# Performance work log

Hardware: AMD Instinct MI355X
Metric: run time of the kernel (lower is better)

## Reference

```python
import jax, jax.numpy as jnp
import numpy as np

N = 50000      # nodes
E = 800000     # edges
G = 2000       # graphs
F_IN = 34
HID = 256
H = 8
D = 32         # HID // H
L = 5


def _layer_norm(x, g, b, eps=1e-5):
    m = x.mean(-1, keepdims=True)
    v = ((x - m) ** 2).mean(-1, keepdims=True)
    return (x - m) / jnp.sqrt(v + eps) * g + b


def _gelu(x):
    return jax.nn.gelu(x, approximate=False)  # torch exact GELU


def _segment_softmax(scores, seg, n):
    # scores: [E', H], seg: [E'] target node ids
    m = jax.ops.segment_max(scores, seg, num_segments=n)
    m = jnp.where(jnp.isfinite(m), m, 0.0)
    ex = jnp.exp(scores - m[seg])
    den = jax.ops.segment_sum(ex, seg, num_segments=n)
    return ex / (den[seg] + 1e-16)


def setup_inputs() -> dict:
    key = jax.random.key(0)
    ks = iter(jax.random.split(key, 64))

    def p(shape, fan):
        return (jax.random.normal(next(ks), shape, jnp.float32) / np.sqrt(fan)).astype(jnp.float32)

    inp = {}
    inp['x'] = jax.random.normal(next(ks), (N, F_IN), jnp.float32)
    inp['edge_index'] = jax.random.randint(next(ks), (2, E), 0, N, jnp.int32)
    inp['batch'] = jnp.sort(jax.random.randint(next(ks), (N,), 0, G, jnp.int32))

    # input embed
    inp['in_W'] = p((F_IN, HID), F_IN); inp['in_b'] = jnp.zeros((HID,), jnp.float32)
    inp['in_ln_g'] = jnp.ones((HID,), jnp.float32); inp['in_ln_b'] = jnp.zeros((HID,), jnp.float32)
    # 5 GATv2 layers (stacked on leading dim)
    inp['gat_Wl'] = p((L, HID, HID), HID); inp['gat_bl'] = jnp.zeros((L, HID), jnp.float32)
    inp['gat_Wr'] = p((L, HID, HID), HID); inp['gat_br'] = jnp.zeros((L, HID), jnp.float32)
    inp['gat_att'] = p((L, H, D), D)
    inp['gat_bias'] = jnp.zeros((L, HID), jnp.float32)
    inp['gat_ln_g'] = jnp.ones((L, HID), jnp.float32); inp['gat_ln_b'] = jnp.zeros((L, HID), jnp.float32)
    # TransformerConv
    inp['tr_Wq'] = p((HID, HID), HID); inp['tr_bq'] = jnp.zeros((HID,), jnp.float32)
    inp['tr_Wk'] = p((HID, HID), HID); inp['tr_bk'] = jnp.zeros((HID,), jnp.float32)
    inp['tr_Wv'] = p((HID, HID), HID); inp['tr_bv'] = jnp.zeros((HID,), jnp.float32)
    inp['tr_Wskip'] = p((HID, HID), HID); inp['tr_bskip'] = jnp.zeros((HID,), jnp.float32)
    inp['tr_ln_g'] = jnp.ones((HID,), jnp.float32); inp['tr_ln_b'] = jnp.zeros((HID,), jnp.float32)
    # output proj
    inp['out_W'] = p((2 * HID, 2 * HID), 2 * HID); inp['out_b'] = jnp.zeros((2 * HID,), jnp.float32)
    inp['out_ln_g'] = jnp.ones((2 * HID,), jnp.float32); inp['out_ln_b'] = jnp.zeros((2 * HID,), jnp.float32)
    return inp


def reference(x, edge_index, batch,
              in_W, in_b, in_ln_g, in_ln_b,
              gat_Wl, gat_bl, gat_Wr, gat_br, gat_att, gat_bias, gat_ln_g, gat_ln_b,
              tr_Wq, tr_bq, tr_Wk, tr_bk, tr_Wv, tr_bv, tr_Wskip, tr_bskip, tr_ln_g, tr_ln_b,
              out_W, out_b, out_ln_g, out_ln_b):
    # input embedding (dropout inactive in eval)
    h = _gelu(_layer_norm(x @ in_W + in_b, in_ln_g, in_ln_b))

    src, dst = edge_index[0], edge_index[1]  # PyG: row=source j, col=target i
    loops = jnp.arange(N, dtype=src.dtype)
    s2 = jnp.concatenate([src, loops])  # GATv2 adds self loops
    d2 = jnp.concatenate([dst, loops])

    for l in range(L):  # small fixed loop over layers
        xl = (h @ gat_Wl[l] + gat_bl[l]).reshape(N, H, D)  # source transform / message
        xr = (h @ gat_Wr[l] + gat_br[l]).reshape(N, H, D)  # target transform
        e = jax.nn.leaky_relu(xl[s2] + xr[d2], 0.2)        # [E', H, D]
        score = jnp.einsum('ehd,hd->eh', e, gat_att[l])
        alpha = _segment_softmax(score, d2, N)             # softmax over incoming edges
        out = jax.ops.segment_sum(xl[s2] * alpha[..., None], d2, num_segments=N)
        out = out.reshape(N, HID) + gat_bias[l]
        h = h + _gelu(_layer_norm(out, gat_ln_g[l], gat_ln_b[l]))

    # TransformerConv (no self loops, root_weight skip connection)
    q = (h @ tr_Wq + tr_bq).reshape(N, H, D)
    k = (h @ tr_Wk + tr_bk).reshape(N, H, D)
    v = (h @ tr_Wv + tr_bv).reshape(N, H, D)
    score = (q[dst] * k[src]).sum(-1) / jnp.sqrt(jnp.float32(D))  # [E, H]
    alpha = _segment_softmax(score, dst, N)
    out = jax.ops.segment_sum(v[src] * alpha[..., None], dst, num_segments=N).reshape(N, HID)
    out = out + h @ tr_Wskip + tr_bskip
    h = h + _layer_norm(out, tr_ln_g, tr_ln_b)

    # global mean + max pool
    cnt = jax.ops.segment_sum(jnp.ones((N,), h.dtype), batch, num_segments=G)
    h_mean = jax.ops.segment_sum(h, batch, num_segments=G) / jnp.maximum(cnt, 1.0)[:, None]
    h_max = jax.ops.segment_max(h, batch, num_segments=G)
    h_max = jnp.where(jnp.isfinite(h_max), h_max, 0.0)
    ge = jnp.concatenate([h_mean, h_max], axis=-1)  # [G, 512]
    return _gelu(_layer_norm(ge @ out_W + out_b, out_ln_g, out_ln_b))
```

## Files before the change

### kernel.cpp

```cpp
#include <hip/hip_runtime.h>
#include <math.h>

#define N_NODES 50000
#define N_EDGES 800000
#define N_GRAPH 2000
#define F_INPUT 34
#define HID 256
#define NLAYER 5

typedef __attribute__((ext_vector_type(8))) short short8;
typedef __attribute__((ext_vector_type(4))) float float4v;

__device__ __forceinline__ float gelu_f(float x) {
  return 0.5f * x * (1.0f + erff(x * 0.70710678118654752440f));
}
__device__ __forceinline__ unsigned short bfr(float f) {
  unsigned u = __float_as_uint(f);
  return (unsigned short)((u + 0x7fffu + ((u >> 16) & 1u)) >> 16);
}
__device__ __forceinline__ float b2f(unsigned short s) {
  return __uint_as_float(((unsigned)s) << 16);
}
__device__ __forceinline__ float4 ld4bf(const unsigned short* p) {
  ushort4 u = *(const ushort4*)p;
  float4 f;
  f.x = b2f(u.x); f.y = b2f(u.y); f.z = b2f(u.z); f.w = b2f(u.w);
  return f;
}
__device__ __forceinline__ void acp16(const unsigned short* g, unsigned short* l) {
  __builtin_amdgcn_global_load_lds(
      (const __attribute__((address_space(1))) void*)g,
      (__attribute__((address_space(3))) void*)l, 16, 0, 0);
}

__global__ __launch_bounds__(256) void gemm_bias(
    const float* __restrict__ A, const float* __restrict__ B,
    const float* __restrict__ bias, float* __restrict__ C,
    int M, int Nn, int K) {
  __shared__ float As[16][64];
  __shared__ float Bs[16][64];
  int tid = threadIdx.x;
  int tx = tid & 15, ty = tid >> 4;
  int row0 = blockIdx.y * 64;
  int col0 = blockIdx.x * 64;
  float acc[4][4] = {};
  int a_r = tid >> 2;
  int a_c = (tid & 3) * 4;
  int b_r = tid >> 4;
  int b_c = (tid & 15) * 4;

  for (int k0 = 0; k0 < K; k0 += 16) {
    int ar = row0 + a_r;
#pragma unroll
    for (int i = 0; i < 4; ++i) {
      int kc = k0 + a_c + i;
      As[a_c + i][a_r] = (ar < M && kc < K) ? A[(long)ar * K + kc] : 0.f;
    }
    int bk = k0 + b_r;
    if (bk < K) {
      float4 bv = *(const float4*)&B[(long)bk * Nn + col0 + b_c];
      Bs[b_r][b_c + 0] = bv.x; Bs[b_r][b_c + 1] = bv.y;
      Bs[b_r][b_c + 2] = bv.z; Bs[b_r][b_c + 3] = bv.w;
    } else {
      Bs[b_r][b_c + 0] = 0.f; Bs[b_r][b_c + 1] = 0.f;
      Bs[b_r][b_c + 2] = 0.f; Bs[b_r][b_c + 3] = 0.f;
    }
    __syncthreads();
#pragma unroll
    for (int kk = 0; kk < 16; ++kk) {
      float4 a = *(const float4*)&As[kk][ty * 4];
      float4 b = *(const float4*)&Bs[kk][tx * 4];
      float av[4] = {a.x, a.y, a.z, a.w};
      float bv[4] = {b.x, b.y, b.z, b.w};
#pragma unroll
      for (int i = 0; i < 4; ++i)
#pragma unroll
        for (int j = 0; j < 4; ++j) acc[i][j] += av[i] * bv[j];
    }
    __syncthreads();
  }
  float4 bi = *(const float4*)&bias[col0 + tx * 4];
  float bia[4] = {bi.x, bi.y, bi.z, bi.w};
#pragma unroll
  for (int i = 0; i < 4; ++i) {
    int r = row0 + ty * 4 + i;
    if (r < M) {
      float4 o;
      o.x = acc[i][0] + bia[0]; o.y = acc[i][1] + bia[1];
      o.z = acc[i][2] + bia[2]; o.w = acc[i][3] + bia[3];
      *(float4*)&C[(long)r * Nn + col0 + tx * 4] = o;
    }
  }
}

__global__ __launch_bounds__(256) void gemm_mfma(
    const unsigned short* __restrict__ A, const unsigned short* __restrict__ Bt,
    const float* __restrict__ bias, void* __restrict__ Cv,
    int M, int Nn, int K, int flags) {
  __shared__ unsigned short smem[12288];
  unsigned short* As = smem;
  unsigned short* Bs = smem + 4096;
  int tid = threadIdx.x;
  int wave = tid >> 6, lane = tid & 63;
  int row0 = blockIdx.y * 128;
  int col0 = blockIdx.x * 128;
  int wm0 = (wave >> 1) * 64;
  int wn0 = (wave & 1) * 64;
  int q = lane >> 4;
  int ln = lane & 15;

  int srow = wave * 16 + (lane >> 2);
  int scol = (lane & 3) * 8;
  int ra0 = min(row0 + srow, M - 1);
  int ra1 = min(row0 + srow + 64, M - 1);
  const unsigned short* pa0 = A + (size_t)ra0 * K + scol;
  const unsigned short* pa1 = A + (size_t)ra1 * K + scol;
  const unsigned short* pb0 = Bt + (size_t)(col0 + srow) * K + scol;
  const unsigned short* pb1 = Bt + (size_t)(col0 + srow + 64) * K + scol;
  unsigned short* la0 = As + wave * 512;
  unsigned short* la1 = As + wave * 512 + 2048;
  unsigned short* lb0 = Bs + wave * 512;
  unsigned short* lb1 = Bs + wave * 512 + 2048;

  float4v acc[4][4];
#pragma unroll
  for (int i = 0; i < 4; ++i)
#pragma unroll
    for (int j = 0; j < 4; ++j) acc[i][j] = (float4v)0.f;

  for (int k0 = 0; k0 < K; k0 += 32) {
    acp16(pa0 + k0, la0);
    acp16(pa1 + k0, la1);
    acp16(pb0 + k0, lb0);
    acp16(pb1 + k0, lb1);
    __syncthreads();
    short8 af[4], bf[4];
#pragma unroll
    for (int i = 0; i < 4; ++i)
      af[i] = *(const short8*)&As[(wm0 + i * 16 + ln) * 32 + q * 8];
#pragma unroll
    for (int j = 0; j < 4; ++j)
      bf[j] = *(const short8*)&Bs[(wn0 + j * 16 + ln) * 32 + q * 8];
#pragma unroll
    for (int i = 0; i < 4; ++i)
#pragma unroll
      for (int j = 0; j < 4; ++j)
        acc[i][j] = __builtin_amdgcn_mfma_f32_16x16x32_bf16(af[i], bf[j], acc[i][j], 0, 0, 0);
    __syncthreads();
  }
  int rb = (lane >> 4) * 4;
  if (flags & 2) {
    unsigned short* Cb = (unsigned short*)Cv;
    unsigned short* eb = smem + wave * 2560;
#pragma unroll
    for (int p = 0; p < 2; ++p) {
#pragma unroll
      for (int jj = 0; jj < 2; ++jj) {
        int j = p * 2 + jj;
        float bv = bias[col0 + wn0 + j * 16 + ln];
#pragma unroll
        for (int i = 0; i < 4; ++i)
#pragma unroll
          for (int r = 0; r < 4; ++r)
            eb[(i * 16 + rb + r) * 40 + jj * 16 + ln] = bfr(acc[i][j][r] + bv);
      }
      int grow = row0 + wm0 + lane;
      uint4 w0 = *(uint4*)&eb[lane * 40 + 0];
      uint4 w1 = *(uint4*)&eb[lane * 40 + 8];
      uint4 w2 = *(uint4*)&eb[lane * 40 + 16];
      uint4 w3 = *(uint4*)&eb[lane * 40 + 24];
      if (grow < M) {
        unsigned short* dst = Cb + (size_t)grow * Nn + col0 + wn0 + p * 32;
        *(uint4*)&dst[0] = w0;
        *(uint4*)&dst[8] = w1;
        *(uint4*)&dst[16] = w2;
        *(uint4*)&dst[24] = w3;
      }
    }
  } else {
    float* C = (float*)Cv;
#pragma unroll
    for (int j = 0; j < 4; ++j) {
      int col = col0 + wn0 + j * 16 + ln;
      float bv = bias[col];
#pragma unroll
      for (int i = 0; i < 4; ++i)
#pragma unroll
        for (int r = 0; r < 4; ++r) {
          int row = row0 + wm0 + i * 16 + rb + r;
          if (row < M) C[(size_t)row * Nn + col] = acc[i][j][r] + bv;
        }
    }
  }
}

__global__ __launch_bounds__(256) void prep_w(
    const float* __restrict__ Wl, const float* __restrict__ Wr,
    const float* __restrict__ Wq, const float* __restrict__ Wk,
    const float* __restrict__ Wv, const float* __restrict__ Wsk,
    unsigned short* __restrict__ out) {
  __shared__ float t[32][33];
  int m = blockIdx.z;
  const float* W = (m < 10) ? (((m & 1) ? Wr : Wl) + (size_t)(m >> 1) * 65536)
                 : (m == 10) ? Wq : (m == 11) ? Wk : (m == 12) ? Wv : Wsk;
  int k0 = blockIdx.y * 32, n0 = blockIdx.x * 32;
  int r = threadIdx.x >> 5, c = threadIdx.x & 31;
  for (int rr = r; rr < 32; rr += 8)
    t[rr][c] = W[(size_t)(k0 + rr) * HID + n0 + c];
  __syncthreads();
  unsigned short* o = out + (size_t)m * 65536;
  for (int rr = r; rr < 32; rr += 8)
    o[(size_t)(n0 + rr) * HID + k0 + c] = bfr(t[c][rr]);
}

__global__ __launch_bounds__(256) void prep_wout(const float* __restrict__ W,
                                                 unsigned short* __restrict__ o) {
  __shared__ float t[32][33];
  int k0 = blockIdx.y * 32, n0 = blockIdx.x * 32;
  int r = threadIdx.x >> 5, c = threadIdx.x & 31;
  for (int rr = r; rr < 32; rr += 8)
    t[rr][c] = W[(size_t)(k0 + rr) * 512 + n0 + c];
  __syncthreads();
  for (int rr = r; rr < 32; rr += 8)
    o[(size_t)(n0 + rr) * 512 + k0 + c] = bfr(t[c][rr]);
}

__global__ __launch_bounds__(256) void prep_bias(
    const float* __restrict__ bl, const float* __restrict__ br,
    const float* __restrict__ bq, const float* __restrict__ bk,
    const float* __restrict__ bv, float* __restrict__ out) {
  int i = blockIdx.x * 256 + threadIdx.x;
  if (i < 2560) {
    int l = i >> 9, c = i & 511;
    out[i] = (c < 256) ? bl[l * 256 + c] : br[l * 256 + (c - 256)];
  } else if (i < 3328) {
    int j = i - 2560;
    out[i] = (j < 256) ? bq[j] : (j < 512) ? bk[j - 256] : bv[j - 512];
  }
}

__global__ __launch_bounds__(256) void ln_act(
    const float* __restrict__ in, const float* __restrict__ gam,
    const float* __restrict__ bet, float* __restrict__ out,
    unsigned short* __restrict__ outb,
    int n_rows, int width, int do_gelu) {
  int wid = blockIdx.x * 4 + (threadIdx.x >> 6);
  int lane = threadIdx.x & 63;
  if (wid >= n_rows) return;
  int chunks = width >> 8;
  float4 v[2];
  float s = 0.f;
  for (int c = 0; c < chunks; ++c) {
    int off = c * 256 + lane * 4;
    float4 t = *(const float4*)&in[(size_t)wid * width + off];
    v[c] = t;
    s += t.x + t.y + t.z + t.w;
  }
  for (int o = 1; o < 64; o <<= 1) s += __shfl_xor(s, o);
  float mean = s / (float)width;
  float vs = 0.f;
  for (int c = 0; c < chunks; ++c) {
    float dx = v[c].x - mean, dy = v[c].y - mean, dz = v[c].z - mean, dw = v[c].w - mean;
    vs += dx * dx + dy * dy + dz * dz + dw * dw;
  }
  for (int o = 1; o < 64; o <<= 1) vs += __shfl_xor(vs, o);
  float inv = rsqrtf(vs / (float)width + 1e-5f);
  for (int c = 0; c < chunks; ++c) {
    int off = c * 256 + lane * 4;
    float4 g4 = *(const float4*)&gam[off];
    float4 b4 = *(const float4*)&bet[off];
    float y[4] = {(v[c].x - mean) * inv * g4.x + b4.x,
                  (v[c].y - mean) * inv * g4.y + b4.y,
                  (v[c].z - mean) * inv * g4.z + b4.z,
                  (v[c].w - mean) * inv * g4.w + b4.w};
    if (do_gelu) {
#pragma unroll
      for (int i = 0; i < 4; ++i) y[i] = gelu_f(y[i]);
    }
    size_t idx = (size_t)wid * width + off;
    float4 o4 = {y[0], y[1], y[2], y[3]};
    *(float4*)&out[idx] = o4;
    if (outb) {
      ushort4 ob = {bfr(y[0]), bfr(y[1]), bfr(y[2]), bfr(y[3])};
      *(ushort4*)&outb[idx] = ob;
    }
  }
}

__global__ __launch_bounds__(256) void edge_count(const int* __restrict__ ei,
                                                  int* __restrict__ counts) {
  int e = blockIdx.x * 256 + threadIdx.x;
  if (e < N_EDGES) atomicAdd(&counts[ei[N_EDGES + e]], 1);
}

__global__ __launch_bounds__(1024) void scan1(const int* __restrict__ counts,
                                              int* __restrict__ indptr,
                                              int* __restrict__ bsums, int n) {
  __shared__ int sm[1024];
  int tid = threadIdx.x;
  int i = blockIdx.x * 1024 + tid;
  int v = (i < n) ? counts[i] : 0;
  sm[tid] = v;
  __syncthreads();
  for (int off = 1; off < 1024; off <<= 1) {
    int t = (tid >= off) ? sm[tid - off] : 0;
    __syncthreads();
    sm[tid] += t;
    __syncthreads();
  }
  if (i < n) indptr[i] = sm[tid] - v;
  if (tid == 1023) bsums[blockIdx.x] = sm[1023];
}

__global__ void scan2(int* __restrict__ bsums, int nb) {
  if (threadIdx.x == 0 && blockIdx.x == 0) {
    int acc = 0;
    for (int i = 0; i < nb; ++i) { int t = bsums[i]; bsums[i] = acc; acc += t; }
  }
}

__global__ __launch_bounds__(256) void scan3(const int* __restrict__ bsums,
                                             int* __restrict__ indptr,
                                             int* __restrict__ cursor, int n) {
  int i = blockIdx.x * 256 + threadIdx.x;
  if (i < n) {
    int v = indptr[i] + bsums[i >> 10];
    indptr[i] = v;
    cursor[i] = v;
  }
  if (i == 0) indptr[n] = N_EDGES;
}

__global__ __launch_bounds__(256) void edge_scatter(const int* __restrict__ ei,
                                                    int* __restrict__ cursor,
                                                    int* __restrict__ esrc) {
  int e = blockIdx.x * 256 + threadIdx.x;
  if (e < N_EDGES) {
    int d = ei[N_EDGES + e];
    int p = atomicAdd(&cursor[d], 1);
    esrc[p] = ei[e];
  }
}

#define GAT_EDGE(f)                                                        \
  {                                                                        \
    float ex = f.x + xri.x; ex = ex > 0.f ? ex : 0.2f * ex;                \
    float ey = f.y + xri.y; ey = ey > 0.f ? ey : 0.2f * ey;                \
    float ez = f.z + xri.z; ez = ez > 0.f ? ez : 0.2f * ez;                \
    float ew = f.w + xri.w; ew = ew > 0.f ? ew : 0.2f * ew;                \
    float p = ex * a4.x + ey * a4.y + ez * a4.z + ew * a4.w;               \
    p += __shfl_xor(p, 1); p += __shfl_xor(p, 2); p += __shfl_xor(p, 4);   \
    float wgt = __expf(fminf(p - m0, 60.f));                               \
    ax += wgt * f.x; ay += wgt * f.y; az += wgt * f.z; aw += wgt * f.w;    \
    lsum += wgt;                                                           \
  }

__global__ __launch_bounds__(256) void gat_agg(
    const unsigned short* __restrict__ xlr, const float* __restrict__ att,
    const int* __restrict__ indptr, const int* __restrict__ esrc,
    const float* __restrict__ pre_bias, const float* __restrict__ gam,
    const float* __restrict__ bet, float* __restrict__ h,
    unsigned short* __restrict__ hb) {
  int wid = blockIdx.x * 4 + (threadIdx.x >> 6);
  int lane = threadIdx.x & 63;
  if (wid >= N_NODES) return;
  size_t idx = (size_t)wid * HID + lane * 4;
  float4 pb = *(const float4*)&pre_bias[lane * 4];
  float4 g4 = *(const float4*)&gam[lane * 4];
  float4 b4 = *(const float4*)&bet[lane * 4];
  float4 r4 = *(const float4*)&h[idx];
  float4 xri = ld4bf(&xlr[(size_t)wid * 512 + 256 + lane * 4]);
  float4 a4 = *(const float4*)&att[lane * 4];
  int beg = indptr[wid], end = indptr[wid + 1];

  float m0, lsum, ax, ay, az, aw;
  {
    float4 f = ld4bf(&xlr[(size_t)wid * 512 + lane * 4]);
    float ex = f.x + xri.x; ex = ex > 0.f ? ex : 0.2f * ex;
    float ey = f.y + xri.y; ey = ey > 0.f ? ey : 0.2f * ey;
    float ez = f.z + xri.z; ez = ez > 0.f ? ez : 0.2f * ez;
    float ew = f.w + xri.w; ew = ew > 0.f ? ew : 0.2f * ew;
    float p = ex * a4.x + ey * a4.y + ez * a4.z + ew * a4.w;
    p += __shfl_xor(p, 1); p += __shfl_xor(p, 2); p += __shfl_xor(p, 4);
    m0 = p; lsum = 1.f;
    ax = f.x; ay = f.y; az = f.z; aw = f.w;
  }
  int e = beg;
  for (; e + 7 < end; e += 8) {
    int j0 = esrc[e],     j1 = esrc[e + 1], j2 = esrc[e + 2], j3 = esrc[e + 3];
    int j4 = esrc[e + 4], j5 = esrc[e + 5], j6 = esrc[e + 6], j7 = esrc[e + 7];
    float4 f0 = ld4bf(&xlr[(size_t)j0 * 512 + lane * 4]);
    float4 f1 = ld4bf(&xlr[(size_t)j1 * 512 + lane * 4]);
    float4 f2 = ld4bf(&xlr[(size_t)j2 * 512 + lane * 4]);
    float4 f3 = ld4bf(&xlr[(size_t)j3 * 512 + lane * 4]);
    float4 f4 = ld4bf(&xlr[(size_t)j4 * 512 + lane * 4]);
    float4 f5 = ld4bf(&xlr[(size_t)j5 * 512 + lane * 4]);
    float4 f6 = ld4bf(&xlr[(size_t)j6 * 512 + lane * 4]);
    float4 f7 = ld4bf(&xlr[(size_t)j7 * 512 + lane * 4]);
    GAT_EDGE(f0); GAT_EDGE(f1); GAT_EDGE(f2); GAT_EDGE(f3);
    GAT_EDGE(f4); GAT_EDGE(f5); GAT_EDGE(f6); GAT_EDGE(f7);
  }
  for (; e + 3 < end; e += 4) {
    int j0 = esrc[e], j1 = esrc[e + 1], j2 = esrc[e + 2], j3 = esrc[e + 3];
    float4 f0 = ld4bf(&xlr[(size_t)j0 * 512 + lane * 4]);
    float4 f1 = ld4bf(&xlr[(size_t)j1 * 512 + lane * 4]);
    float4 f2 = ld4bf(&xlr[(size_t)j2 * 512 + lane * 4]);
    float4 f3 = ld4bf(&xlr[(size_t)j3 * 512 + lane * 4]);
    GAT_EDGE(f0); GAT_EDGE(f1); GAT_EDGE(f2); GAT_EDGE(f3);
  }
  for (; e < end; ++e) {
    int j = esrc[e];
    float4 f = ld4bf(&xlr[(size_t)j * 512 + lane * 4]);
    GAT_EDGE(f);
  }
  float inv = 1.f / (lsum + 1e-16f);
  float y0 = ax * inv + pb.x, y1 = ay * inv + pb.y;
  float y2 = az * inv + pb.z, y3 = aw * inv + pb.w;
  float s = y0 + y1 + y2 + y3;
  for (int o = 1; o < 64; o <<= 1) s += __shfl_xor(s, o);
  float mean = s * (1.f / 256.f);
  float d0 = y0 - mean, d1 = y1 - mean, d2 = y2 - mean, d3 = y3 - mean;
  float vs = d0 * d0 + d1 * d1 + d2 * d2 + d3 * d3;
  for (int o = 1; o < 64; o <<= 1) vs += __shfl_xor(vs, o);
  float inv2 = rsqrtf(vs * (1.f / 256.f) + 1e-5f);
  y0 = gelu_f(d0 * inv2 * g4.x + b4.x) + r4.x;
  y1 = gelu_f(d1 * inv2 * g4.y + b4.y) + r4.y;
  y2 = gelu_f(d2 * inv2 * g4.z + b4.z) + r4.z;
  y3 = gelu_f(d3 * inv2 * g4.w + b4.w) + r4.w;
  float4 o4 = {y0, y1, y2, y3};
  *(float4*)&h[idx] = o4;
  ushort4 ob = {bfr(y0), bfr(y1), bfr(y2), bfr(y3)};
  *(ushort4*)&hb[idx] = ob;
}

#define TR_EDGE(kj, vj)                                                    \
  {                                                                        \
    float p = qi.x * kj.x + qi.y * kj.y + qi.z * kj.z + qi.w * kj.w;       \
    p += __shfl_xor(p, 1); p += __shfl_xor(p, 2); p += __shfl_xor(p, 4);   \
    float wgt = __expf(fminf(p * scale, 60.f));                            \
    ax += wgt * vj.x; ay += wgt * vj.y; az += wgt * vj.z; aw += wgt * vj.w;\
    lsum += wgt;                                                           \
  }

__global__ __launch_bounds__(256) void tr_agg(
    const unsigned short* __restrict__ qkv, const int* __restrict__ indptr,
    const int* __restrict__ esrc, const unsigned short* __restrict__ skipb,
    const float* __restrict__ gam, const float* __restrict__ bet,
    float* __restrict__ h) {
  int wid = blockIdx.x * 4 + (threadIdx.x >> 6);
  int lane = threadIdx.x & 63;
  if (wid >= N_NODES) return;
  size_t idx = (size_t)wid * HID + lane * 4;
  float4 sk = ld4bf(&skipb[idx]);
  float4 g4 = *(const float4*)&gam[lane * 4];
  float4 b4 = *(const float4*)&bet[lane * 4];
  float4 r4 = *(const float4*)&h[idx];
  float4 qi = ld4bf(&qkv[(size_t)wid * 768 + lane * 4]);
  int beg = indptr[wid], end = indptr[wid + 1];
  float lsum = 0.f;
  float ax = 0.f, ay = 0.f, az = 0.f, aw = 0.f;
  const float scale = 0.17677669529663687f;
  int e = beg;
  for (; e + 3 < end; e += 4) {
    int j0 = esrc[e], j1 = esrc[e + 1], j2 = esrc[e + 2], j3 = esrc[e + 3];
    float4 k0 = ld4bf(&qkv[(size_t)j0 * 768 + 256 + lane * 4]);
    float4 v0 = ld4bf(&qkv[(size_t)j0 * 768 + 512 + lane * 4]);
    float4 k1 = ld4bf(&qkv[(size_t)j1 * 768 + 256 + lane * 4]);
    float4 v1 = ld4bf(&qkv[(size_t)j1 * 768 + 512 + lane * 4]);
    float4 k2 = ld4bf(&qkv[(size_t)j2 * 768 + 256 + lane * 4]);
    float4 v2 = ld4bf(&qkv[(size_t)j2 * 768 + 512 + lane * 4]);
    float4 k3 = ld4bf(&qkv[(size_t)j3 * 768 + 256 + lane * 4]);
    float4 v3 = ld4bf(&qkv[(size_t)j3 * 768 + 512 + lane * 4]);
    TR_EDGE(k0, v0); TR_EDGE(k1, v1); TR_EDGE(k2, v2); TR_EDGE(k3, v3);
  }
  for (; e < end; ++e) {
    int j = esrc[e];
    float4 kj = ld4bf(&qkv[(size_t)j * 768 + 256 + lane * 4]);
    float4 vj = ld4bf(&qkv[(size_t)j * 768 + 512 + lane * 4]);
    TR_EDGE(kj, vj);
  }
  float inv = 1.f / (lsum + 1e-16f);
  float y0 = ax * inv + sk.x, y1 = ay * inv + sk.y;
  float y2 = az * inv + sk.z, y3 = aw * inv + sk.w;
  float s = y0 + y1 + y2 + y3;
  for (int o = 1; o < 64; o <<= 1) s += __shfl_xor(s, o);
  float mean = s * (1.f / 256.f);
  float d0 = y0 - mean, d1 = y1 - mean, d2 = y2 - mean, d3 = y3 - mean;
  float vs = d0 * d0 + d1 * d1 + d2 * d2 + d3 * d3;
  for (int o = 1; o < 64; o <<= 1) vs += __shfl_xor(vs, o);
  float inv2 = rsqrtf(vs * (1.f / 256.f) + 1e-5f);
  float4 o4;
  o4.x = r4.x + d0 * inv2 * g4.x + b4.x;
  o4.y = r4.y + d1 * inv2 * g4.y + b4.y;
  o4.z = r4.z + d2 * inv2 * g4.z + b4.z;
  o4.w = r4.w + d3 * inv2 * g4.w + b4.w;
  *(float4*)&h[idx] = o4;
}

__global__ __launch_bounds__(256) void graph_bounds(const int* __restrict__ batch,
                                                    int* __restrict__ gptr) {
  int i = blockIdx.x * 256 + threadIdx.x;
  if (i >= N_NODES) return;
  int b0 = batch[i];
  if (i == 0)
    for (int g = 0; g <= b0; ++g) gptr[g] = 0;
  int b1 = (i + 1 < N_NODES) ? batch[i + 1] : N_GRAPH;
  for (int g = b0 + 1; g <= b1; ++g) gptr[g] = i + 1;
}

__global__ __launch_bounds__(256) void pool_seg(
    const float* __restrict__ h, const int* __restrict__ gptr,
    unsigned short* __restrict__ geb) {
  int g = blockIdx.x, c = threadIdx.x;
  int s = gptr[g], e = gptr[g + 1];
  float sum = 0.f, mx = -INFINITY;
  for (int r = s; r < e; ++r) {
    float vv = h[(size_t)r * HID + c];
    sum += vv;
    mx = fmaxf(mx, vv);
  }
  int cnt = e - s;
  geb[(size_t)g * 512 + c] = bfr(sum / (float)max(cnt, 1));
  geb[(size_t)g * 512 + 256 + c] = bfr(cnt ? mx : 0.f);
}

static inline void mfma_launch(const unsigned short* A, const unsigned short* Bt,
                               const float* bias, void* C, int M, int Nn, int K,
                               int flags, hipStream_t s) {
  dim3 grid(Nn / 128, (M + 127) / 128);
  gemm_mfma<<<grid, 256, 0, s>>>(A, Bt, bias, C, M, Nn, K, flags);
}

extern "C" void kernel_launch(void* const* d_in, const int* in_sizes, int n_in,
                              void* d_out, int out_size, void* d_ws, size_t ws_size,
                              hipStream_t stream) {
  const float* x       = (const float*)d_in[0];
  const int*   ei      = (const int*)d_in[1];
  const int*   batch   = (const int*)d_in[2];
  const float* in_W    = (const float*)d_in[3];
  const float* in_b    = (const float*)d_in[4];
  const float* in_ln_g = (const float*)d_in[5];
  const float* in_ln_b = (const float*)d_in[6];
  const float* gat_Wl  = (const float*)d_in[7];
  const float* gat_bl  = (const float*)d_in[8];
  const float* gat_Wr  = (const float*)d_in[9];
  const float* gat_br  = (const float*)d_in[10];
  const float* gat_att = (const float*)d_in[11];
  const float* gat_bias= (const float*)d_in[12];
  const float* gat_ln_g= (const float*)d_in[13];
  const float* gat_ln_b= (const float*)d_in[14];
  const float* tr_Wq   = (const float*)d_in[15];
  const float* tr_bq   = (const float*)d_in[16];
  const float* tr_Wk   = (const float*)d_in[17];
  const float* tr_bk   = (const float*)d_in[18];
  const float* tr_Wv   = (const float*)d_in[19];
  const float* tr_bv   = (const float*)d_in[20];
  const float* tr_Wsk  = (const float*)d_in[21];
  const float* tr_bsk  = (const float*)d_in[22];
  const float* tr_ln_g = (const float*)d_in[23];
  const float* tr_ln_b = (const float*)d_in[24];
  const float* out_W   = (const float*)d_in[25];
  const float* out_b   = (const float*)d_in[26];
  const float* out_ln_g= (const float*)d_in[27];
  const float* out_ln_b= (const float*)d_in[28];

  char* w = (char*)d_ws;
  auto take = [&](size_t bytes) -> char* {
    char* p = w;
    w += (bytes + 255) & ~(size_t)255;
    return p;
  };
  const size_t NB = (size_t)N_NODES * HID * sizeof(float);
  float* h    = (float*)take(NB);
  float* aggO = (float*)take(NB);
  unsigned short* hb  = (unsigned short*)take((size_t)N_NODES * HID * 2);
  unsigned short* xq  = (unsigned short*)take((size_t)N_NODES * 768 * 2);
  unsigned short* wbuf= (unsigned short*)take((size_t)(14 * 65536 + 262144) * 2);
  float* bcat = (float*)take(3328 * sizeof(float));
  int* indptr = (int*)take((N_NODES + 1) * sizeof(int));
  int* cursor = (int*)take(N_NODES * sizeof(int));
  int* counts = (int*)take(N_NODES * sizeof(int));
  int* esrc   = (int*)take(N_EDGES * sizeof(int));
  int* bsums  = (int*)take(64 * sizeof(int));
  unsigned short* skipb = (unsigned short*)aggO;
  char* w2 = (char*)xq;
  auto take2 = [&](size_t bytes) -> char* {
    char* p = w2;
    w2 += (bytes + 255) & ~(size_t)255;
    return p;
  };
  int* gptr = (int*)take2((N_GRAPH + 1) * sizeof(int));
  unsigned short* geb = (unsigned short*)take2((size_t)N_GRAPH * 512 * 2);
  float* tbuf = (float*)take2((size_t)N_GRAPH * 512 * sizeof(float));

  const int EB = (N_EDGES + 255) / 256;
  const int WB = (N_NODES + 3) / 4;
  const int NSB = (N_NODES + 1023) / 1024;

  {
    dim3 g(8, 8, 14);
    prep_w<<<g, 256, 0, stream>>>(gat_Wl, gat_Wr, tr_Wq, tr_Wk, tr_Wv, tr_Wsk, wbuf);
    dim3 g2(16, 16);
    prep_wout<<<g2, 256, 0, stream>>>(out_W, wbuf + (size_t)14 * 65536);
    prep_bias<<<13, 256, 0, stream>>>(gat_bl, gat_br, tr_bq, tr_bk, tr_bv, bcat);
  }

  hipMemsetAsync(counts, 0, N_NODES * sizeof(int), stream);
  edge_count<<<EB, 256, 0, stream>>>(ei, counts);
  scan1<<<NSB, 1024, 0, stream>>>(counts, indptr, bsums, N_NODES);
  scan2<<<1, 64, 0, stream>>>(bsums, NSB);
  scan3<<<(N_NODES + 255) / 256, 256, 0, stream>>>(bsums, indptr, cursor, N_NODES);
  edge_scatter<<<EB, 256, 0, stream>>>(ei, cursor, esrc);

  {
    dim3 grid(HID / 64, (N_NODES + 63) / 64);
    gemm_bias<<<grid, 256, 0, stream>>>(x, in_W, in_b, aggO, N_NODES, HID, F_INPUT);
  }
  ln_act<<<WB, 256, 0, stream>>>(aggO, in_ln_g, in_ln_b, h, hb, N_NODES, HID, 1);

  for (int l = 0; l < NLAYER; ++l) {
    mfma_launch(hb, wbuf + (size_t)(2 * l) * 65536, bcat + l * 512, xq,
                N_NODES, 512, HID, 2, stream);
    gat_agg<<<WB, 256, 0, stream>>>(xq, gat_att + l * HID, indptr, esrc,
                                    gat_bias + l * HID, gat_ln_g + l * HID,
                                    gat_ln_b + l * HID, h, hb);
  }

  mfma_launch(hb, wbuf + (size_t)13 * 65536, tr_bsk, skipb,
              N_NODES, HID, HID, 2, stream);
  mfma_launch(hb, wbuf + (size_t)10 * 65536, bcat + 2560, xq,
              N_NODES, 768, HID, 2, stream);
  tr_agg<<<WB, 256, 0, stream>>>(xq, indptr, esrc, skipb, tr_ln_g, tr_ln_b, h);

  graph_bounds<<<(N_NODES + 255) / 256, 256, 0, stream>>>(batch, gptr);
  pool_seg<<<N_GRAPH, 256, 0, stream>>>(h, gptr, geb);

  mfma_launch(geb, wbuf + (size_t)14 * 65536, out_b, tbuf,
              N_GRAPH, 512, 512, 0, stream);
  ln_act<<<(N_GRAPH + 3) / 4, 256, 0, stream>>>(tbuf, out_ln_g, out_ln_b,
                                                (float*)d_out, nullptr,
                                                N_GRAPH, 512, 1);
}
```

Before: 1.274 ms.

## Interleave K/V weights, split transformer edges across wave pairs, drop tiny kernels

Reorders the K and V weight rows and biases so each lane's K and V values for a source node sit together, letting one 16-byte load fetch both. Each node in tr_agg is now handled by two waves that take alternate edges and combine partial sums through shared memory. The separate scan2 and graph_bounds kernels are removed: scan3 sums the block totals itself, and pool_seg finds graph bounds by binary search over batch. Loads of the LN, bias and residual parameters in gat_agg are moved after the edge loop to shorten register live ranges. The price is an extra block barrier in tr_agg and redundant bound searches across blocks.

```diff
diff --git a/kernel.cpp b/kernel.cpp
--- a/kernel.cpp
+++ b/kernel.cpp
@@ -26,6 +26,10 @@
   float4 f;
   f.x = b2f(u.x); f.y = b2f(u.y); f.z = b2f(u.z); f.w = b2f(u.w);
   return f;
+}
+__device__ __forceinline__ void unpk(unsigned u, float& a, float& b) {
+  a = __uint_as_float(u << 16);
+  b = __uint_as_float(u & 0xffff0000u);
 }
 __device__ __forceinline__ void acp16(const unsigned short* g, unsigned short* l) {
   __builtin_amdgcn_global_load_lds(
@@ -208,9 +212,22 @@
   for (int rr = r; rr < 32; rr += 8)
     t[rr][c] = W[(size_t)(k0 + rr) * HID + n0 + c];
   __syncthreads();
-  unsigned short* o = out + (size_t)m * 65536;
-  for (int rr = r; rr < 32; rr += 8)
-    o[(size_t)(n0 + rr) * HID + k0 + c] = bfr(t[c][rr]);
+  for (int rr = r; rr < 32; rr += 8) {
+    int n = n0 + rr;
+    unsigned short* o;
+    int drow;
+    if (m == 11) {
+      o = out + (size_t)10 * 65536;
+      drow = 256 + (n >> 2) * 8 + (n & 3);
+    } else if (m == 12) {
+      o = out + (size_t)10 * 65536;
+      drow = 256 + (n >> 2) * 8 + 4 + (n & 3);
+    } else {
+      o = out + (size_t)m * 65536;
+      drow = n;
+    }
+    o[(size_t)drow * HID + k0 + c] = bfr(t[c][rr]);
+  }
 }
 
 __global__ __launch_bounds__(256) void prep_wout(const float* __restrict__ W,
@@ -235,7 +252,12 @@
     out[i] = (c < 256) ? bl[l * 256 + c] : br[l * 256 + (c - 256)];
   } else if (i < 3328) {
     int j = i - 2560;
-    out[i] = (j < 256) ? bq[j] : (j < 512) ? bk[j - 256] : bv[j - 512];
+    if (j < 256) {
+      out[i] = bq[j];
+    } else {
+      int t = j - 256, g = t >> 3, r = t & 7;
+      out[i] = (r < 4) ? bk[4 * g + r] : bv[4 * g + (r - 4)];
+    }
   }
 }
 
@@ -312,19 +334,15 @@
   if (tid == 1023) bsums[blockIdx.x] = sm[1023];
 }
 
-__global__ void scan2(int* __restrict__ bsums, int nb) {
-  if (threadIdx.x == 0 && blockIdx.x == 0) {
-    int acc = 0;
-    for (int i = 0; i < nb; ++i) { int t = bsums[i]; bsums[i] = acc; acc += t; }
-  }
-}
-
 __global__ __launch_bounds__(256) void scan3(const int* __restrict__ bsums,
                                              int* __restrict__ indptr,
                                              int* __restrict__ cursor, int n) {
   int i = blockIdx.x * 256 + threadIdx.x;
+  int blk = blockIdx.x >> 2;
+  int off = 0;
+  for (int b = 0; b < blk; ++b) off += bsums[b];
   if (i < n) {
-    int v = indptr[i] + bsums[i >> 10];
+    int v = indptr[i] + off;
     indptr[i] = v;
     cursor[i] = v;
   }
@@ -364,11 +382,6 @@
   int wid = blockIdx.x * 4 + (threadIdx.x >> 6);
   int lane = threadIdx.x & 63;
   if (wid >= N_NODES) return;
-  size_t idx = (size_t)wid * HID + lane * 4;
-  float4 pb = *(const float4*)&pre_bias[lane * 4];
-  float4 g4 = *(const float4*)&gam[lane * 4];
-  float4 b4 = *(const float4*)&bet[lane * 4];
-  float4 r4 = *(const float4*)&h[idx];
   float4 xri = ld4bf(&xlr[(size_t)wid * 512 + 256 + lane * 4]);
   float4 a4 = *(const float4*)&att[lane * 4];
   int beg = indptr[wid], end = indptr[wid + 1];
@@ -414,6 +427,7 @@
     GAT_EDGE(f);
   }
   float inv = 1.f / (lsum + 1e-16f);
+  float4 pb = *(const float4*)&pre_bias[lane * 4];
   float y0 = ax * inv + pb.x, y1 = ay * inv + pb.y;
   float y2 = az * inv + pb.z, y3 = aw * inv + pb.w;
   float s = y0 + y1 + y2 + y3;
@@ -423,6 +437,10 @@
   float vs = d0 * d0 + d1 * d1 + d2 * d2 + d3 * d3;
   for (int o = 1; o < 64; o <<= 1) vs += __shfl_xor(vs, o);
   float inv2 = rsqrtf(vs * (1.f / 256.f) + 1e-5f);
+  float4 g4 = *(const float4*)&gam[lane * 4];
+  float4 b4 = *(const float4*)&bet[lane * 4];
+  size_t idx = (size_t)wid * HID + lane * 4;
+  float4 r4 = *(const float4*)&h[idx];
   y0 = gelu_f(d0 * inv2 * g4.x + b4.x) + r4.x;
   y1 = gelu_f(d1 * inv2 * g4.y + b4.y) + r4.y;
   y2 = gelu_f(d2 * inv2 * g4.z + b4.z) + r4.z;
@@ -433,12 +451,15 @@
   *(ushort4*)&hb[idx] = ob;
 }
 
-#define TR_EDGE(kj, vj)                                                    \
+#define TR_EDGE_I(u)                                                       \
   {                                                                        \
-    float p = qi.x * kj.x + qi.y * kj.y + qi.z * kj.z + qi.w * kj.w;       \
+    float kx, ky, kz, kw, vx, vy, vz, vw;                                  \
+    unpk(u.x, kx, ky); unpk(u.y, kz, kw);                                  \
+    unpk(u.z, vx, vy); unpk(u.w, vz, vw);                                  \
+    float p = qi.x * kx + qi.y * ky + qi.z * kz + qi.w * kw;               \
     p += __shfl_xor(p, 1); p += __shfl_xor(p, 2); p += __shfl_xor(p, 4);   \
     float wgt = __expf(fminf(p * scale, 60.f));                            \
-    ax += wgt * vj.x; ay += wgt * vj.y; az += wgt * vj.z; aw += wgt * vj.w;\
+    ax += wgt * vx; ay += wgt * vy; az += wgt * vz; aw += wgt * vw;        \
     lsum += wgt;                                                           \
   }
 
@@ -447,39 +468,44 @@
     const int* __restrict__ esrc, const unsigned short* __restrict__ skipb,
     const float* __restrict__ gam, const float* __restrict__ bet,
     float* __restrict__ h) {
-  int wid = blockIdx.x * 4 + (threadIdx.x >> 6);
-  int lane = threadIdx.x & 63;
-  if (wid >= N_NODES) return;
-  size_t idx = (size_t)wid * HID + lane * 4;
-  float4 sk = ld4bf(&skipb[idx]);
-  float4 g4 = *(const float4*)&gam[lane * 4];
-  float4 b4 = *(const float4*)&bet[lane * 4];
-  float4 r4 = *(const float4*)&h[idx];
+  __shared__ float comb[2][5][64];
+  int tid = threadIdx.x;
+  int wave = tid >> 6, lane = tid & 63;
+  int pair = wave >> 1, half = wave & 1;
+  int wid = blockIdx.x * 2 + pair;
   float4 qi = ld4bf(&qkv[(size_t)wid * 768 + lane * 4]);
   int beg = indptr[wid], end = indptr[wid + 1];
   float lsum = 0.f;
   float ax = 0.f, ay = 0.f, az = 0.f, aw = 0.f;
   const float scale = 0.17677669529663687f;
-  int e = beg;
-  for (; e + 3 < end; e += 4) {
-    int j0 = esrc[e], j1 = esrc[e + 1], j2 = esrc[e + 2], j3 = esrc[e + 3];
-    float4 k0 = ld4bf(&qkv[(size_t)j0 * 768 + 256 + lane * 4]);
-    float4 v0 = ld4bf(&qkv[(size_t)j0 * 768 + 512 + lane * 4]);
-    float4 k1 = ld4bf(&qkv[(size_t)j1 * 768 + 256 + lane * 4]);
-    float4 v1 = ld4bf(&qkv[(size_t)j1 * 768 + 512 + lane * 4]);
-    float4 k2 = ld4bf(&qkv[(size_t)j2 * 768 + 256 + lane * 4]);
-    float4 v2 = ld4bf(&qkv[(size_t)j2 * 768 + 512 + lane * 4]);
-    float4 k3 = ld4bf(&qkv[(size_t)j3 * 768 + 256 + lane * 4]);
-    float4 v3 = ld4bf(&qkv[(size_t)j3 * 768 + 512 + lane * 4]);
-    TR_EDGE(k0, v0); TR_EDGE(k1, v1); TR_EDGE(k2, v2); TR_EDGE(k3, v3);
-  }
-  for (; e < end; ++e) {
+  int e = beg + half;
+  for (; e + 6 < end; e += 8) {
+    int j0 = esrc[e], j1 = esrc[e + 2], j2 = esrc[e + 4], j3 = esrc[e + 6];
+    uint4 u0 = *(const uint4*)&qkv[(size_t)j0 * 768 + 256 + lane * 8];
+    uint4 u1 = *(const uint4*)&qkv[(size_t)j1 * 768 + 256 + lane * 8];
+    uint4 u2 = *(const uint4*)&qkv[(size_t)j2 * 768 + 256 + lane * 8];
+    uint4 u3 = *(const uint4*)&qkv[(size_t)j3 * 768 + 256 + lane * 8];
+    TR_EDGE_I(u0); TR_EDGE_I(u1); TR_EDGE_I(u2); TR_EDGE_I(u3);
+  }
+  for (; e < end; e += 2) {
     int j = esrc[e];
-    float4 kj = ld4bf(&qkv[(size_t)j * 768 + 256 + lane * 4]);
-    float4 vj = ld4bf(&qkv[(size_t)j * 768 + 512 + lane * 4]);
-    TR_EDGE(kj, vj);
-  }
+    uint4 u = *(const uint4*)&qkv[(size_t)j * 768 + 256 + lane * 8];
+    TR_EDGE_I(u);
+  }
+  if (half) {
+    comb[pair][0][lane] = ax; comb[pair][1][lane] = ay;
+    comb[pair][2][lane] = az; comb[pair][3][lane] = aw;
+    comb[pair][4][lane] = lsum;
+  }
+  __syncthreads();
+  if (half) return;
+  ax += comb[pair][0][lane]; ay += comb[pair][1][lane];
+  az += comb[pair][2][lane]; aw += comb[pair][3][lane];
+  lsum += comb[pair][4][lane];
+
   float inv = 1.f / (lsum + 1e-16f);
+  size_t idx = (size_t)wid * HID + lane * 4;
+  float4 sk = ld4bf(&skipb[idx]);
   float y0 = ax * inv + sk.x, y1 = ay * inv + sk.y;
   float y2 = az * inv + sk.z, y3 = aw * inv + sk.w;
   float s = y0 + y1 + y2 + y3;
@@ -489,6 +515,9 @@
   float vs = d0 * d0 + d1 * d1 + d2 * d2 + d3 * d3;
   for (int o = 1; o < 64; o <<= 1) vs += __shfl_xor(vs, o);
   float inv2 = rsqrtf(vs * (1.f / 256.f) + 1e-5f);
+  float4 g4 = *(const float4*)&gam[lane * 4];
+  float4 b4 = *(const float4*)&bet[lane * 4];
+  float4 r4 = *(const float4*)&h[idx];
   float4 o4;
   o4.x = r4.x + d0 * inv2 * g4.x + b4.x;
   o4.y = r4.y + d1 * inv2 * g4.y + b4.y;
@@ -497,22 +526,16 @@
   *(float4*)&h[idx] = o4;
 }
 
-__global__ __launch_bounds__(256) void graph_bounds(const int* __restrict__ batch,
-                                                    int* __restrict__ gptr) {
-  int i = blockIdx.x * 256 + threadIdx.x;
-  if (i >= N_NODES) return;
-  int b0 = batch[i];
-  if (i == 0)
-    for (int g = 0; g <= b0; ++g) gptr[g] = 0;
-  int b1 = (i + 1 < N_NODES) ? batch[i + 1] : N_GRAPH;
-  for (int g = b0 + 1; g <= b1; ++g) gptr[g] = i + 1;
-}
-
 __global__ __launch_bounds__(256) void pool_seg(
-    const float* __restrict__ h, const int* __restrict__ gptr,
+    const float* __restrict__ h, const int* __restrict__ batch,
     unsigned short* __restrict__ geb) {
   int g = blockIdx.x, c = threadIdx.x;
-  int s = gptr[g], e = gptr[g + 1];
+  int lo = 0, hi = N_NODES;
+  while (lo < hi) { int mid = (lo + hi) >> 1; if (batch[mid] < g) lo = mid + 1; else hi = mid; }
+  int s = lo;
+  hi = N_NODES;
+  while (lo < hi) { int mid = (lo + hi) >> 1; if (batch[mid] < g + 1) lo = mid + 1; else hi = mid; }
+  int e = lo;
   float sum = 0.f, mx = -INFINITY;
   for (int r = s; r < e; ++r) {
     float vv = h[(size_t)r * HID + c];
@@ -589,12 +612,12 @@
     w2 += (bytes + 255) & ~(size_t)255;
     return p;
   };
-  int* gptr = (int*)take2((N_GRAPH + 1) * sizeof(int));
   unsigned short* geb = (unsigned short*)take2((size_t)N_GRAPH * 512 * 2);
   float* tbuf = (float*)take2((size_t)N_GRAPH * 512 * sizeof(float));
 
   const int EB = (N_EDGES + 255) / 256;
   const int WB = (N_NODES + 3) / 4;
+  const int WB2 = N_NODES / 2;
   const int NSB = (N_NODES + 1023) / 1024;
 
   {
@@ -608,7 +631,6 @@
   hipMemsetAsync(counts, 0, N_NODES * sizeof(int), stream);
   edge_count<<<EB, 256, 0, stream>>>(ei, counts);
   scan1<<<NSB, 1024, 0, stream>>>(counts, indptr, bsums, N_NODES);
-  scan2<<<1, 64, 0, stream>>>(bsums, NSB);
   scan3<<<(N_NODES + 255) / 256, 256, 0, stream>>>(bsums, indptr, cursor, N_NODES);
   edge_scatter<<<EB, 256, 0, stream>>>(ei, cursor, esrc);
 
@@ -630,10 +652,9 @@
               N_NODES, HID, HID, 2, stream);
   mfma_launch(hb, wbuf + (size_t)10 * 65536, bcat + 2560, xq,
               N_NODES, 768, HID, 2, stream);
-  tr_agg<<<WB, 256, 0, stream>>>(xq, indptr, esrc, skipb, tr_ln_g, tr_ln_b, h);
-
-  graph_bounds<<<(N_NODES + 255) / 256, 256, 0, stream>>>(batch, gptr);
-  pool_seg<<<N_GRAPH, 256, 0, stream>>>(h, gptr, geb);
+  tr_agg<<<WB2, 256, 0, stream>>>(xq, indptr, esrc, skipb, tr_ln_g, tr_ln_b, h);
+
+  pool_seg<<<N_GRAPH, 256, 0, stream>>>(h, batch, geb);
 
   mfma_launch(geb, wbuf + (size_t)14 * 65536, out_b, tbuf,
               N_GRAPH, 512, 512, 0, stream);
```

Result: faster. 1.195 ms (-6.2%).
